# Optimization experiments

Hardware: AMD Instinct MI355X
Metric: run time of the kernel (lower is better)

Reference implementation:

```python
import jax, jax.numpy as jnp
from jax import lax
import numpy as np

B, T, D_IN, H, OUT = 256, 336, 64, 256, 1


def _lstm_dir(x, w_ih, w_hh, b_ih, b_hh, reverse):
    """Single-direction LSTM over x: [B, T, D] -> hidden seq [B, T, H].
    PyTorch gate order: i, f, g, o along the 4H axis."""
    Bx = x.shape[0]
    Hd = w_hh.shape[1]
    # Precompute input projections for all timesteps: [T, B, 4H]
    xg = jnp.einsum('btd,gd->tbg', x, w_ih) + b_ih + b_hh

    def step(carry, xg_t):
        h, c = carry
        g = xg_t + h @ w_hh.T  # [B, 4H]
        i, f, gg, o = jnp.split(g, 4, axis=-1)
        i = jax.nn.sigmoid(i)
        f = jax.nn.sigmoid(f)
        gg = jnp.tanh(gg)
        o = jax.nn.sigmoid(o)
        c = f * c + i * gg
        h = o * jnp.tanh(c)
        return (h, c), h

    h0 = jnp.zeros((Bx, Hd), x.dtype)
    _, hs = lax.scan(step, (h0, h0), xg, reverse=reverse)  # hs aligned with t
    return jnp.swapaxes(hs, 0, 1)  # [B, T, H]


def _bilstm_layer(x, pf, pr):
    h_f = _lstm_dir(x, *pf, reverse=False)
    h_r = _lstm_dir(x, *pr, reverse=True)
    return jnp.concatenate([h_f, h_r], axis=-1)  # [B, T, 2H]


def setup_inputs() -> dict:
    key = jax.random.key(0)
    ks = jax.random.split(key, 20)
    s = 1.0 / np.sqrt(H)  # PyTorch default init scale
    u = lambda k, shape: jax.random.uniform(k, shape, jnp.float32, -s, s)
    d = {
        'x': jax.random.normal(ks[0], (B, T, D_IN), jnp.float32),
        'w_ih_l0': u(ks[1], (4 * H, D_IN)), 'w_hh_l0': u(ks[2], (4 * H, H)),
        'b_ih_l0': u(ks[3], (4 * H,)), 'b_hh_l0': u(ks[4], (4 * H,)),
        'w_ih_l0r': u(ks[5], (4 * H, D_IN)), 'w_hh_l0r': u(ks[6], (4 * H, H)),
        'b_ih_l0r': u(ks[7], (4 * H,)), 'b_hh_l0r': u(ks[8], (4 * H,)),
        'w_ih_l1': u(ks[9], (4 * H, 2 * H)), 'w_hh_l1': u(ks[10], (4 * H, H)),
        'b_ih_l1': u(ks[11], (4 * H,)), 'b_hh_l1': u(ks[12], (4 * H,)),
        'w_ih_l1r': u(ks[13], (4 * H, 2 * H)), 'w_hh_l1r': u(ks[14], (4 * H, H)),
        'b_ih_l1r': u(ks[15], (4 * H,)), 'b_hh_l1r': u(ks[16], (4 * H,)),
        'fc_w': u(ks[17], (OUT, 2 * H)), 'fc_b': u(ks[18], (OUT,)),
    }
    return d


def reference(x, w_ih_l0, w_hh_l0, b_ih_l0, b_hh_l0,
              w_ih_l0r, w_hh_l0r, b_ih_l0r, b_hh_l0r,
              w_ih_l1, w_hh_l1, b_ih_l1, b_hh_l1,
              w_ih_l1r, w_hh_l1r, b_ih_l1r, b_hh_l1r,
              fc_w, fc_b):
    h = _bilstm_layer(x, (w_ih_l0, w_hh_l0, b_ih_l0, b_hh_l0),
                      (w_ih_l0r, w_hh_l0r, b_ih_l0r, b_hh_l0r))
    h = _bilstm_layer(h, (w_ih_l1, w_hh_l1, b_ih_l1, b_hh_l1),
                      (w_ih_l1r, w_hh_l1r, b_ih_l1r, b_hh_l1r))
    last = h[:, -1, :]  # [B, 2H]
    return last @ fc_w.T + fc_b  # [B, OUT]
```

## Files before the change

### kernel.cpp

```cpp
#include <hip/hip_runtime.h>
#include <stdint.h>

#define TT 336
#define BB 256

typedef __attribute__((ext_vector_type(8))) short short8;
typedef __attribute__((ext_vector_type(4))) float f32x4;
typedef __attribute__((ext_vector_type(4))) float float4v;
typedef __attribute__((ext_vector_type(2))) unsigned long long ull2;

__device__ __forceinline__ uint16_t f2bf(float f){
    uint32_t u = __builtin_bit_cast(uint32_t, f);
    u += 0x7fffu + ((u >> 16) & 1u);
    return (uint16_t)(u >> 16);
}
__device__ __forceinline__ float bf2f(uint16_t h){
    uint32_t u = ((uint32_t)h) << 16;
    return __builtin_bit_cast(float, u);
}
__device__ __forceinline__ float sigf(float x){
    return __fdividef(1.0f, 1.0f + __expf(-x));
}
__device__ __forceinline__ float tanhf_f(float x){
    return __fdividef(2.0f, 1.0f + __expf(-2.0f * x)) - 1.0f;
}

__global__ void prepack(const float* __restrict__ w_ih_l0, const float* __restrict__ w_hh_l0,
                        const float* __restrict__ w_ih_l0r, const float* __restrict__ w_hh_l0r,
                        const float* __restrict__ w_hh_l1, const float* __restrict__ w_ih_l1,
                        const float* __restrict__ b_ih_l0, const float* __restrict__ b_hh_l0,
                        const float* __restrict__ b_ih_l0r, const float* __restrict__ b_hh_l0r,
                        const float* __restrict__ b_ih_l1, const float* __restrict__ b_hh_l1,
                        uint16_t* __restrict__ Wp_l0f, uint16_t* __restrict__ Wp_l0r,
                        uint16_t* __restrict__ Wp_l1f, uint16_t* __restrict__ Wp_ih1,
                        float* __restrict__ bias)
{
    const int which = blockIdx.y;
    const int idx = blockIdx.x * 256 + threadIdx.x;
    if (which < 2) {
        if (idx >= 64*10*64*8) return;
        int e = idx & 7, lane = (idx >> 3) & 63, rem = idx >> 9;
        int kf = rem % 10, tile = rem / 10;
        int col = tile*16 + (lane & 15);
        int k   = kf*32 + (lane >> 4)*8 + e;
        const float* wi = which ? w_ih_l0r : w_ih_l0;
        const float* wh = which ? w_hh_l0r : w_hh_l0;
        float v = (k < 64) ? wi[col*64 + k] : wh[col*256 + (k - 64)];
        (which ? Wp_l0r : Wp_l0f)[idx] = f2bf(v);
    } else if (which == 2) {
        if (idx >= 64*8*64*8) return;
        int e = idx & 7, lane = (idx >> 3) & 63, rem = idx >> 9;
        int kf = rem & 7, tile = rem >> 3;
        int col = tile*16 + (lane & 15);
        int k   = kf*32 + (lane >> 4)*8 + e;
        Wp_l1f[idx] = f2bf(w_hh_l1[col*256 + k]);
    } else if (which == 3) {
        if (idx >= 64*16*64*8) return;
        int e = idx & 7, lane = (idx >> 3) & 63, rem = idx >> 9;
        int kf = rem & 15, tile = rem >> 4;
        int col = tile*16 + (lane & 15);
        int k   = kf*32 + (lane >> 4)*8 + e;
        Wp_ih1[idx] = f2bf(w_ih_l1[col*512 + k]);
    } else {
        if (idx >= 3072) return;
        int j = idx & 1023;
        float v = (idx < 1024) ? (b_ih_l0[j] + b_hh_l0[j])
                : (idx < 2048) ? (b_ih_l0r[j] + b_hh_l0r[j])
                               : (b_ih_l1[j] + b_hh_l1[j]);
        bias[idx] = v;
    }
}

__global__ void zero_flags(uint32_t* __restrict__ flags) {
    if (threadIdx.x < 96) flags[threadIdx.x] = 0;
}

template<int LAYER>
__global__ __launch_bounds__(512, 2) void scan_pair(
    const float* __restrict__ x,
    const uint16_t* __restrict__ WpF,
    const uint16_t* __restrict__ WpR,
    const float* __restrict__ bias2,
    const uint16_t* __restrict__ xg,
    uint16_t* __restrict__ l0out,
    float* __restrict__ hlast,
    uint16_t* __restrict__ exch,
    uint32_t* __restrict__ flags)
{
    constexpr int KF  = (LAYER == 0) ? 10 : 8;
    constexpr int KH0 = (LAYER == 0) ? 2 : 0;

    const int tid  = threadIdx.x;
    const int lane = tid & 63, wv = tid >> 6;
    const int lrow = lane & 15, lkg = lane >> 4;
    const int bid  = blockIdx.x;
    const int m    = bid & 1;
    const int pairId = bid >> 1;
    int dir, mch;
    if (LAYER == 0) { dir = pairId >> 4; mch = pairId & 15; }
    else            { dir = 0;           mch = pairId; }
    const int b0   = mch * 16;
    const int hd0  = m * 128;
    const int dimLocal = wv * 16 + lrow;

    const uint16_t* Wp = (LAYER == 0 && dir) ? WpR : WpF;
    const char* wlane = (const char*)Wp + (size_t)lane * 16;
    short8 wfx[4][2];
    short8 wfo[4][4];
    short8 wfp[4][4];
    #pragma unroll
    for (int g = 0; g < 4; ++g) {
        const int tile = g*16 + m*8 + wv;
        if (LAYER == 0) {
            #pragma unroll
            for (int k = 0; k < 2; ++k)
                wfx[g][k] = *(const short8*)(wlane + (size_t)(tile*KF + k) * 1024);
        }
        #pragma unroll
        for (int j = 0; j < 4; ++j) {
            wfo[g][j] = *(const short8*)(wlane + (size_t)(tile*KF + KH0 + m*4 + j) * 1024);
            wfp[g][j] = *(const short8*)(wlane + (size_t)(tile*KF + KH0 + (1-m)*4 + j) * 1024);
        }
    }

    float biasreg[4];
    if (LAYER == 0) {
        const float* bs = bias2 + dir * 1024;
        #pragma unroll
        for (int g = 0; g < 4; ++g)
            biasreg[g] = bs[g*256 + hd0 + dimLocal];
    }

    uint16_t* exMine = exch + (size_t)bid * 4096;
    const uint16_t* exPart = exch + (size_t)(bid ^ 1) * 4096;
    uint32_t* fMine = flags + bid;
    uint32_t* fPart = flags + (bid ^ 1);

    __shared__ __align__(16) uint16_t hb[16 * 128];
    __shared__ __align__(16) uint16_t xb[16 * 64];
    char* hbc = (char*)hb;
    char* xbc = (char*)xb;

    ((uint64_t*)hb)[tid] = 0ull;
    ((uint64_t*)exMine)[tid] = 0ull;

    if (LAYER == 0 && tid < 256) {
        const int t0 = dir ? (TT - 1) : 0;
        const int row = tid >> 4, k0 = (tid & 15) * 4;
        float4v v = *(const float4v*)(x + ((size_t)(b0 + row) * TT + t0) * 64 + k0);
        uint32_t lo = (uint32_t)f2bf(v[0]) | ((uint32_t)f2bf(v[1]) << 16);
        uint32_t hi = (uint32_t)f2bf(v[2]) | ((uint32_t)f2bf(v[3]) << 16);
        int a = (row*128 + k0*2) ^ ((row & 7) << 4);
        *(uint32_t*)(xbc + a)     = lo;
        *(uint32_t*)(xbc + a + 4) = hi;
    }

    uint2 xgv[4], xgn[4];
    if (LAYER == 1) {
        #pragma unroll
        for (int g = 0; g < 4; ++g) {
            const int tile = g*16 + m*8 + wv;
            xgv[g] = *(const uint2*)((const char*)xg + ((size_t)mch * 64 + tile) * 512 + (size_t)lane * 8);
        }
    }

    float cst[4];
    #pragma unroll
    for (int i = 0; i < 4; ++i) cst[i] = 0.0f;

    __syncthreads();
    if (tid == 0)
        __hip_atomic_store(fMine, 1u, __ATOMIC_RELEASE, __HIP_MEMORY_SCOPE_AGENT);

    for (int step = 0; step < TT; ++step) {
        const int t = (LAYER == 0 && dir) ? (TT - 1 - step) : step;

        f32x4 acc[4];
        if (LAYER == 0) {
            #pragma unroll
            for (int g = 0; g < 4; ++g) {
                float bv = biasreg[g];
                acc[g] = (f32x4){bv, bv, bv, bv};
            }
        } else {
            #pragma unroll
            for (int g = 0; g < 4; ++g) {
                uint2 v = xgv[g];
                acc[g][0] = bf2f((uint16_t)(v.x & 0xffffu));
                acc[g][1] = bf2f((uint16_t)(v.x >> 16));
                acc[g][2] = bf2f((uint16_t)(v.y & 0xffffu));
                acc[g][3] = bf2f((uint16_t)(v.y >> 16));
            }
        }

        if (LAYER == 0) {
            #pragma unroll
            for (int kf = 0; kf < 2; ++kf) {
                int a = (lrow*128 + (kf*32 + lkg*8)*2) ^ ((lrow & 7) << 4);
                short8 av = *(const short8*)(xbc + a);
                #pragma unroll
                for (int g = 0; g < 4; ++g)
                    acc[g] = __builtin_amdgcn_mfma_f32_16x16x32_bf16(av, wfx[g][kf], acc[g], 0, 0, 0);
            }
        }
        #pragma unroll
        for (int j = 0; j < 4; ++j) {
            int a = (lrow*256 + (j*32 + lkg*8)*2) ^ ((lrow & 7) << 4);
            short8 av = *(const short8*)(hbc + a);
            #pragma unroll
            for (int g = 0; g < 4; ++g)
                acc[g] = __builtin_amdgcn_mfma_f32_16x16x32_bf16(av, wfo[g][j], acc[g], 0, 0, 0);
        }

        float4v xload;
        const bool do_x = (LAYER == 0) && (step + 1 < TT);
        if (do_x && tid < 256) {
            const int tn = dir ? (t - 1) : (t + 1);
            const int row = tid >> 4, k0 = (tid & 15) * 4;
            xload = *(const float4v*)(x + ((size_t)(b0 + row) * TT + tn) * 64 + k0);
        }
        if (LAYER == 1 && step + 1 < TT) {
            #pragma unroll
            for (int g = 0; g < 4; ++g) {
                const int tile = g*16 + m*8 + wv;
                xgn[g] = *(const uint2*)((const char*)xg + ((size_t)((step + 1) * 16 + mch) * 64 + tile) * 512 + (size_t)lane * 8);
            }
        }

        if (tid == 0) {
            while (__hip_atomic_load(fPart, __ATOMIC_RELAXED, __HIP_MEMORY_SCOPE_AGENT) < (uint32_t)(step + 1)) {}
            (void)__hip_atomic_load(fPart, __ATOMIC_ACQUIRE, __HIP_MEMORY_SCOPE_AGENT);
        }
        __syncthreads();
        {
            const uint16_t* ep = exPart + (size_t)(step & 1) * 2048;
            #pragma unroll
            for (int j = 0; j < 4; ++j) {
                const unsigned long long* q =
                    (const unsigned long long*)(ep + j*512 + lane*8);
                ull2 tv;
                tv[0] = __hip_atomic_load(q,     __ATOMIC_RELAXED, __HIP_MEMORY_SCOPE_AGENT);
                tv[1] = __hip_atomic_load(q + 1, __ATOMIC_RELAXED, __HIP_MEMORY_SCOPE_AGENT);
                short8 av = __builtin_bit_cast(short8, tv);
                #pragma unroll
                for (int g = 0; g < 4; ++g)
                    acc[g] = __builtin_amdgcn_mfma_f32_16x16x32_bf16(av, wfp[g][j], acc[g], 0, 0, 0);
            }
        }

        const int kfr = dimLocal >> 5, rem = dimLocal & 31;
        uint16_t* exw = exMine + (size_t)((step + 1) & 1) * 2048 + kfr*512 + (rem >> 3)*128 + (rem & 7);
        #pragma unroll
        for (int r = 0; r < 4; ++r) {
            float iv = sigf(acc[0][r]);
            float fv = sigf(acc[1][r]);
            float gv = tanhf_f(acc[2][r]);
            float ov = sigf(acc[3][r]);
            float cn = fv * cst[r] + iv * gv;
            cst[r] = cn;
            float hv = ov * tanhf_f(cn);
            uint16_t hbits = f2bf(hv);
            const int row = lkg*4 + r;
            *(uint16_t*)(hbc + ((row*256 + dimLocal*2) ^ ((row & 7) << 4))) = hbits;
            if (step + 1 < TT)
                __hip_atomic_store((unsigned short*)(exw + row * 8), (unsigned short)hbits,
                                   __ATOMIC_RELAXED, __HIP_MEMORY_SCOPE_AGENT);
            if (LAYER == 0) {
                l0out[((size_t)t * 256 + (size_t)(b0 + row)) * 512 + dir*256 + hd0 + dimLocal] = hbits;
            } else if (step == TT - 1) {
                hlast[(size_t)(b0 + row) * 256 + hd0 + dimLocal] = hv;
            }
        }

        if (do_x && tid < 256) {
            const int row = tid >> 4, k0 = (tid & 15) * 4;
            uint32_t lo = (uint32_t)f2bf(xload[0]) | ((uint32_t)f2bf(xload[1]) << 16);
            uint32_t hi = (uint32_t)f2bf(xload[2]) | ((uint32_t)f2bf(xload[3]) << 16);
            int a = (row*128 + k0*2) ^ ((row & 7) << 4);
            *(uint32_t*)(xbc + a)     = lo;
            *(uint32_t*)(xbc + a + 4) = hi;
        }
        if (LAYER == 1) {
            #pragma unroll
            for (int g = 0; g < 4; ++g) xgv[g] = xgn[g];
        }

        __syncthreads();
        if (tid == 0 && step + 1 < TT)
            __hip_atomic_store(fMine, (uint32_t)(step + 2), __ATOMIC_RELEASE, __HIP_MEMORY_SCOPE_AGENT);
    }
}

__global__ __launch_bounds__(256, 2) void gemm_xg1(
    const uint16_t* __restrict__ l0out,
    const uint16_t* __restrict__ Wp,
    const float* __restrict__ bias,
    uint16_t* __restrict__ xg1p)
{
    __shared__ __align__(16) uint16_t ab[64 * 512];
    char* abc = (char*)ab;
    const int tid = threadIdx.x;
    const int lane = tid & 63, wv = tid >> 6;
    const int lrow = lane & 15, lkg = lane >> 4;
    const int wg = blockIdx.x;
    const size_t rowbase = (size_t)wg * 64;

    #pragma unroll
    for (int i = 0; i < 16; ++i) {
        int cch = tid + i * 256;
        int row = cch >> 6, kc = cch & 63;
        short8 v = *(const short8*)(l0out + (rowbase + row) * 512 + kc * 8);
        int a = (row*1024 + kc*16) ^ ((row & 7) << 4);
        *(short8*)(abc + a) = v;
    }
    __syncthreads();

    float biasreg[16];
    #pragma unroll
    for (int j = 0; j < 16; ++j) biasreg[j] = bias[wv*256 + j*16 + lrow];

    const char* wlane = (const char*)Wp + (size_t)lane * 16;

    for (int j = 0; j < 16; ++j) {
        const int tile = wv*16 + j;
        short8 wfr[16];
        #pragma unroll
        for (int kf = 0; kf < 16; ++kf)
            wfr[kf] = *(const short8*)(wlane + (size_t)(tile*16 + kf) * 1024);
        f32x4 acc[4];
        #pragma unroll
        for (int mt = 0; mt < 4; ++mt) {
            float bv = biasreg[j];
            acc[mt] = (f32x4){bv, bv, bv, bv};
        }
        #pragma unroll
        for (int kf = 0; kf < 16; ++kf) {
            #pragma unroll
            for (int mt = 0; mt < 4; ++mt) {
                int row = mt*16 + lrow;
                int a = (row*1024 + kf*64 + lkg*16) ^ ((row & 7) << 4);
                short8 av = *(const short8*)(abc + a);
                acc[mt] = __builtin_amdgcn_mfma_f32_16x16x32_bf16(av, wfr[kf], acc[mt], 0, 0, 0);
            }
        }
        #pragma unroll
        for (int mt = 0; mt < 4; ++mt) {
            uint2 o;
            o.x = (uint32_t)f2bf(acc[mt][0]) | ((uint32_t)f2bf(acc[mt][1]) << 16);
            o.y = (uint32_t)f2bf(acc[mt][2]) | ((uint32_t)f2bf(acc[mt][3]) << 16);
            *(uint2*)((char*)xg1p + ((size_t)(wg*4 + mt) * 64 + tile) * 512 + (size_t)lane * 8) = o;
        }
    }
}

__global__ __launch_bounds__(256) void l1r_fc(
    const uint16_t* __restrict__ l0out,
    const float* __restrict__ w_ih,
    const float* __restrict__ b_ih,
    const float* __restrict__ b_hh,
    const float* __restrict__ hlast,
    const float* __restrict__ fc_w,
    const float* __restrict__ fc_b,
    float* __restrict__ out)
{
    __shared__ __align__(16) float x1[512];
    __shared__ float red[256];
    const int tid = threadIdx.x;
    const int b = blockIdx.x;
    for (int i = tid; i < 512; i += 256)
        x1[i] = bf2f(l0out[((size_t)(TT - 1) * 256 + b) * 512 + i]);
    __syncthreads();
    float di = b_ih[tid]       + b_hh[tid];
    float dg = b_ih[512 + tid] + b_hh[512 + tid];
    float dv = b_ih[768 + tid] + b_hh[768 + tid];
    const float4v* wi = (const float4v*)(w_ih + (size_t)tid * 512);
    const float4v* wg = (const float4v*)(w_ih + (size_t)(512 + tid) * 512);
    const float4v* wo = (const float4v*)(w_ih + (size_t)(768 + tid) * 512);
    for (int k = 0; k < 128; ++k) {
        float4v xv = *(const float4v*)(x1 + k * 4);
        float4v a = wi[k], bq = wg[k], cq = wo[k];
        di += a[0]*xv[0] + a[1]*xv[1] + a[2]*xv[2] + a[3]*xv[3];
        dg += bq[0]*xv[0] + bq[1]*xv[1] + bq[2]*xv[2] + bq[3]*xv[3];
        dv += cq[0]*xv[0] + cq[1]*xv[1] + cq[2]*xv[2] + cq[3]*xv[3];
    }
    float cv = sigf(di) * tanhf_f(dg);
    float hr = sigf(dv) * tanhf_f(cv);
    float pcontrib = fc_w[tid] * hlast[(size_t)b * 256 + tid] + fc_w[256 + tid] * hr;
    red[tid] = pcontrib;
    __syncthreads();
    #pragma unroll
    for (int s = 128; s > 0; s >>= 1) {
        if (tid < s) red[tid] += red[tid + s];
        __syncthreads();
    }
    if (tid == 0) out[b] = red[0] + fc_b[0];
}

extern "C" void kernel_launch(void* const* d_in, const int* in_sizes, int n_in,
                              void* d_out, int out_size, void* d_ws, size_t ws_size,
                              hipStream_t stream)
{
    const float* x        = (const float*)d_in[0];
    const float* w_ih_l0  = (const float*)d_in[1];
    const float* w_hh_l0  = (const float*)d_in[2];
    const float* b_ih_l0  = (const float*)d_in[3];
    const float* b_hh_l0  = (const float*)d_in[4];
    const float* w_ih_l0r = (const float*)d_in[5];
    const float* w_hh_l0r = (const float*)d_in[6];
    const float* b_ih_l0r = (const float*)d_in[7];
    const float* b_hh_l0r = (const float*)d_in[8];
    const float* w_ih_l1  = (const float*)d_in[9];
    const float* w_hh_l1  = (const float*)d_in[10];
    const float* b_ih_l1  = (const float*)d_in[11];
    const float* b_hh_l1  = (const float*)d_in[12];
    const float* w_ih_l1r = (const float*)d_in[13];
    const float* b_ih_l1r = (const float*)d_in[15];
    const float* b_hh_l1r = (const float*)d_in[16];
    const float* fc_w     = (const float*)d_in[17];
    const float* fc_b     = (const float*)d_in[18];
    float* out = (float*)d_out;
    (void)in_sizes; (void)n_in; (void)out_size; (void)ws_size;

    char* p = (char*)d_ws;
    size_t o = 0;
    auto take = [&](size_t bytes) -> char* {
        char* r = p + o; o += (bytes + 255) & ~(size_t)255; return r;
    };
    uint16_t* Wp_l0f = (uint16_t*)take(64*10*64*8 * 2);
    uint16_t* Wp_l0r = (uint16_t*)take(64*10*64*8 * 2);
    uint16_t* Wp_l1f = (uint16_t*)take(64*8*64*8 * 2);
    uint16_t* Wp_ih1 = (uint16_t*)take(64*16*64*8 * 2);
    float*    bias   = (float*)take(3 * 1024 * 4);
    uint16_t* l0out  = (uint16_t*)take((size_t)TT*BB*512*2);
    uint16_t* xg1p   = (uint16_t*)take((size_t)TT*16*64*64*4*2);
    float*    hlast  = (float*)take(BB * 256 * 4);
    uint32_t* flags  = (uint32_t*)take(96 * 4);
    uint16_t* exch0  = (uint16_t*)take((size_t)64 * 4096 * 2);
    uint16_t* exch1  = (uint16_t*)take((size_t)32 * 4096 * 2);

    zero_flags<<<1, 128, 0, stream>>>(flags);

    prepack<<<dim3(2048, 5, 1), 256, 0, stream>>>(
        w_ih_l0, w_hh_l0, w_ih_l0r, w_hh_l0r, w_hh_l1, w_ih_l1,
        b_ih_l0, b_hh_l0, b_ih_l0r, b_hh_l0r, b_ih_l1, b_hh_l1,
        Wp_l0f, Wp_l0r, Wp_l1f, Wp_ih1, bias);

    scan_pair<0><<<64, 512, 0, stream>>>(x, Wp_l0f, Wp_l0r, bias, nullptr,
                                         l0out, nullptr, exch0, flags);

    gemm_xg1<<<(TT * BB) / 64, 256, 0, stream>>>(l0out, Wp_ih1, bias + 2048, xg1p);

    scan_pair<1><<<32, 512, 0, stream>>>(nullptr, Wp_l1f, nullptr, nullptr, xg1p,
                                         nullptr, hlast, exch1, flags + 64);

    l1r_fc<<<BB, 256, 0, stream>>>(l0out, w_ih_l1r, b_ih_l1r, b_hh_l1r, hlast, fc_w, fc_b, out);
}
```

Measured before the change: 3.762 ms.

## Double-buffer LDS hidden state and vectorize partner exchange and l0out stores

Double-buffers the shared hidden-state tile so each step reads one buffer and writes the other. Every wave now spins on the partner flag itself through readfirstlane, which removes the block barrier before the exchange read. The scalar 16-bit atomic stores to the exchange buffer and the scalar layer-0 output writes become 64-bit vector stores issued from LDS after one barrier. Empty asm constraints pin the weight fragments in registers. The risks are heavier flag polling traffic from all waves and a different memory ordering of exchange writes relative to the flag release.

After: 5.215 ms. +38.6%, slower.

```diff
diff --git a/kernel.cpp b/kernel.cpp
--- a/kernel.cpp
+++ b/kernel.cpp
@@ -72,7 +72,7 @@
 }
 
 __global__ void zero_flags(uint32_t* __restrict__ flags) {
-    if (threadIdx.x < 96) flags[threadIdx.x] = 0;
+    if (threadIdx.x < 128) flags[threadIdx.x] = 0;
 }
 
 template<int LAYER>
@@ -122,6 +122,13 @@
             wfp[g][j] = *(const short8*)(wlane + (size_t)(tile*KF + KH0 + (1-m)*4 + j) * 1024);
         }
     }
+    #pragma unroll
+    for (int g = 0; g < 4; ++g) {
+        if (LAYER == 0)
+            asm volatile("" : "+v"(wfx[g][0]), "+v"(wfx[g][1]));
+        asm volatile("" : "+v"(wfo[g][0]), "+v"(wfo[g][1]), "+v"(wfo[g][2]), "+v"(wfo[g][3]));
+        asm volatile("" : "+v"(wfp[g][0]), "+v"(wfp[g][1]), "+v"(wfp[g][2]), "+v"(wfp[g][3]));
+    }
 
     float biasreg[4];
     if (LAYER == 0) {
@@ -136,13 +143,13 @@
     uint32_t* fMine = flags + bid;
     uint32_t* fPart = flags + (bid ^ 1);
 
-    __shared__ __align__(16) uint16_t hb[16 * 128];
+    __shared__ __align__(16) uint16_t hb[2][16 * 128];
     __shared__ __align__(16) uint16_t xb[16 * 64];
-    char* hbc = (char*)hb;
     char* xbc = (char*)xb;
 
     ((uint64_t*)hb)[tid] = 0ull;
-    ((uint64_t*)exMine)[tid] = 0ull;
+    __hip_atomic_store((uint64_t*)exMine + tid, 0ull,
+                       __ATOMIC_RELAXED, __HIP_MEMORY_SCOPE_AGENT);
 
     if (LAYER == 0 && tid < 256) {
         const int t0 = dir ? (TT - 1) : 0;
@@ -174,6 +181,8 @@
 
     for (int step = 0; step < TT; ++step) {
         const int t = (LAYER == 0 && dir) ? (TT - 1 - step) : step;
+        char* hbRc = (char*)hb + (size_t)(step & 1) * 4096;
+        char* hbWc = (char*)hb + (size_t)((step + 1) & 1) * 4096;
 
         f32x4 acc[4];
         if (LAYER == 0) {
@@ -181,6 +190,14 @@
             for (int g = 0; g < 4; ++g) {
                 float bv = biasreg[g];
                 acc[g] = (f32x4){bv, bv, bv, bv};
+            }
+            #pragma unroll
+            for (int kf = 0; kf < 2; ++kf) {
+                int a = (lrow*128 + (kf*32 + lkg*8)*2) ^ ((lrow & 7) << 4);
+                short8 av = *(const short8*)(xbc + a);
+                #pragma unroll
+                for (int g = 0; g < 4; ++g)
+                    acc[g] = __builtin_amdgcn_mfma_f32_16x16x32_bf16(av, wfx[g][kf], acc[g], 0, 0, 0);
             }
         } else {
             #pragma unroll
@@ -192,21 +209,10 @@
                 acc[g][3] = bf2f((uint16_t)(v.y >> 16));
             }
         }
-
-        if (LAYER == 0) {
-            #pragma unroll
-            for (int kf = 0; kf < 2; ++kf) {
-                int a = (lrow*128 + (kf*32 + lkg*8)*2) ^ ((lrow & 7) << 4);
-                short8 av = *(const short8*)(xbc + a);
-                #pragma unroll
-                for (int g = 0; g < 4; ++g)
-                    acc[g] = __builtin_amdgcn_mfma_f32_16x16x32_bf16(av, wfx[g][kf], acc[g], 0, 0, 0);
-            }
-        }
         #pragma unroll
         for (int j = 0; j < 4; ++j) {
             int a = (lrow*256 + (j*32 + lkg*8)*2) ^ ((lrow & 7) << 4);
-            short8 av = *(const short8*)(hbc + a);
+            short8 av = *(const short8*)(hbRc + a);
             #pragma unroll
             for (int g = 0; g < 4; ++g)
                 acc[g] = __builtin_amdgcn_mfma_f32_16x16x32_bf16(av, wfo[g][j], acc[g], 0, 0, 0);
@@ -227,29 +233,35 @@
             }
         }
 
-        if (tid == 0) {
-            while (__hip_atomic_load(fPart, __ATOMIC_RELAXED, __HIP_MEMORY_SCOPE_AGENT) < (uint32_t)(step + 1)) {}
+        {
+            const uint32_t target = (uint32_t)(step + 1);
+            while ((uint32_t)__builtin_amdgcn_readfirstlane(
+                    (int)__hip_atomic_load(fPart, __ATOMIC_RELAXED, __HIP_MEMORY_SCOPE_AGENT)) < target) {}
             (void)__hip_atomic_load(fPart, __ATOMIC_ACQUIRE, __HIP_MEMORY_SCOPE_AGENT);
         }
-        __syncthreads();
         {
-            const uint16_t* ep = exPart + (size_t)(step & 1) * 2048;
+            const char* ep = (const char*)exPart + (size_t)(step & 1) * 4096;
+            const uint64_t* q = (const uint64_t*)(ep + (size_t)lane * 16);
+            uint64_t w[8];
             #pragma unroll
             for (int j = 0; j < 4; ++j) {
-                const unsigned long long* q =
-                    (const unsigned long long*)(ep + j*512 + lane*8);
-                ull2 tv;
-                tv[0] = __hip_atomic_load(q,     __ATOMIC_RELAXED, __HIP_MEMORY_SCOPE_AGENT);
-                tv[1] = __hip_atomic_load(q + 1, __ATOMIC_RELAXED, __HIP_MEMORY_SCOPE_AGENT);
-                short8 av = __builtin_bit_cast(short8, tv);
-                #pragma unroll
-                for (int g = 0; g < 4; ++g)
-                    acc[g] = __builtin_amdgcn_mfma_f32_16x16x32_bf16(av, wfp[g][j], acc[g], 0, 0, 0);
-            }
-        }
-
-        const int kfr = dimLocal >> 5, rem = dimLocal & 31;
-        uint16_t* exw = exMine + (size_t)((step + 1) & 1) * 2048 + kfr*512 + (rem >> 3)*128 + (rem & 7);
+                w[2*j]   = __hip_atomic_load(q + j*128,     __ATOMIC_RELAXED, __HIP_MEMORY_SCOPE_AGENT);
+                w[2*j+1] = __hip_atomic_load(q + j*128 + 1, __ATOMIC_RELAXED, __HIP_MEMORY_SCOPE_AGENT);
+            }
+            ull2 t0 = {w[0], w[1]}, t1 = {w[2], w[3]}, t2 = {w[4], w[5]}, t3 = {w[6], w[7]};
+            short8 av0 = __builtin_bit_cast(short8, t0);
+            short8 av1 = __builtin_bit_cast(short8, t1);
+            short8 av2 = __builtin_bit_cast(short8, t2);
+            short8 av3 = __builtin_bit_cast(short8, t3);
+            #pragma unroll
+            for (int g = 0; g < 4; ++g) {
+                acc[g] = __builtin_amdgcn_mfma_f32_16x16x32_bf16(av0, wfp[g][0], acc[g], 0, 0, 0);
+                acc[g] = __builtin_amdgcn_mfma_f32_16x16x32_bf16(av1, wfp[g][1], acc[g], 0, 0, 0);
+                acc[g] = __builtin_amdgcn_mfma_f32_16x16x32_bf16(av2, wfp[g][2], acc[g], 0, 0, 0);
+                acc[g] = __builtin_amdgcn_mfma_f32_16x16x32_bf16(av3, wfp[g][3], acc[g], 0, 0, 0);
+            }
+        }
+
         #pragma unroll
         for (int r = 0; r < 4; ++r) {
             float iv = sigf(acc[0][r]);
@@ -259,19 +271,26 @@
             float cn = fv * cst[r] + iv * gv;
             cst[r] = cn;
             float hv = ov * tanhf_f(cn);
-            uint16_t hbits = f2bf(hv);
             const int row = lkg*4 + r;
-            *(uint16_t*)(hbc + ((row*256 + dimLocal*2) ^ ((row & 7) << 4))) = hbits;
-            if (step + 1 < TT)
-                __hip_atomic_store((unsigned short*)(exw + row * 8), (unsigned short)hbits,
-                                   __ATOMIC_RELAXED, __HIP_MEMORY_SCOPE_AGENT);
-            if (LAYER == 0) {
-                l0out[((size_t)t * 256 + (size_t)(b0 + row)) * 512 + dir*256 + hd0 + dimLocal] = hbits;
-            } else if (step == TT - 1) {
+            *(uint16_t*)(hbWc + ((row*256 + dimLocal*2) ^ ((row & 7) << 4))) = f2bf(hv);
+            if (LAYER == 1 && step == TT - 1)
                 hlast[(size_t)(b0 + row) * 256 + hd0 + dimLocal] = hv;
-            }
-        }
-
+        }
+
+        __syncthreads();
+
+        if (step + 1 < TT) {
+            const int r  = (tid >> 1) & 15;
+            const int d  = (tid >> 7) * 32 + ((tid >> 5) & 3) * 8 + (tid & 1) * 4;
+            uint64_t v = *(const uint64_t*)(hbWc + ((r*256 + d*2) ^ ((r & 7) << 4)));
+            uint64_t* dst = (uint64_t*)(exMine + (size_t)((step + 1) & 1) * 2048) + tid;
+            __hip_atomic_store(dst, v, __ATOMIC_RELAXED, __HIP_MEMORY_SCOPE_AGENT);
+        }
+        if (LAYER == 0) {
+            const int row = tid >> 5, d4 = (tid & 31) * 4;
+            uint64_t v = *(const uint64_t*)(hbWc + ((row*256 + d4*2) ^ ((row & 7) << 4)));
+            *(uint64_t*)(l0out + ((size_t)t * 256 + (size_t)(b0 + row)) * 512 + dir*256 + hd0 + d4) = v;
+        }
         if (do_x && tid < 256) {
             const int row = tid >> 4, k0 = (tid & 15) * 4;
             uint32_t lo = (uint32_t)f2bf(xload[0]) | ((uint32_t)f2bf(xload[1]) << 16);
@@ -434,7 +453,7 @@
     uint16_t* l0out  = (uint16_t*)take((size_t)TT*BB*512*2);
     uint16_t* xg1p   = (uint16_t*)take((size_t)TT*16*64*64*4*2);
     float*    hlast  = (float*)take(BB * 256 * 4);
-    uint32_t* flags  = (uint32_t*)take(96 * 4);
+    uint32_t* flags  = (uint32_t*)take(128 * 4);
     uint16_t* exch0  = (uint16_t*)take((size_t)64 * 4096 * 2);
     uint16_t* exch1  = (uint16_t*)take((size_t)32 * 4096 * 2);
 
```
